# Kernel optimization log

Measured on AMD Instinct MI355X. Metric: run time of the kernel, lower is better.

The kernel has to match this reference:

```python
import jax, jax.numpy as jnp
import numpy as np

WIN = 3  # window_size (stride fixed to 1, matching module defaults)


def setup_inputs() -> dict:
    key = jax.random.key(0)
    ks = jax.random.split(key, 5)
    B, D, L = 4, 768, 4096
    s = 1.0 / np.sqrt(D)  # PyTorch nn.RNN init: U(-1/sqrt(hidden), 1/sqrt(hidden))
    return {
        "x": jax.random.normal(ks[0], (B, D, L), dtype=jnp.float32),
        "W_ih": jax.random.uniform(ks[1], (D, D), jnp.float32, -s, s),
        "W_hh": jax.random.uniform(ks[2], (D, D), jnp.float32, -s, s),
        "b_ih": jax.random.uniform(ks[3], (D,), jnp.float32, -s, s),
        "b_hh": jax.random.uniform(ks[4], (D,), jnp.float32, -s, s),
        "gamma": jnp.ones((L,), jnp.float32),  # LayerNorm over length axis
        "beta": jnp.zeros((L,), jnp.float32),
    }


def reference(x, W_ih, W_hh, b_ih, b_hh, gamma, beta):
    # x: [B, D, L]. For each position i, run a 1-layer ReLU RNN (h0=0) over the
    B, D, L = x.shape
    xt = jnp.transpose(x, (2, 0, 1))  # [L, B, D] (seq-first, like the torch code)
    xp = jnp.concatenate([jnp.zeros((WIN - 1, B, D), x.dtype), xt], axis=0)  # left-pad
    idx = jnp.arange(L)[:, None] + jnp.arange(WIN)[None, :]
    win = xp[idx]
    valid = (jnp.arange(L)[:, None] - (WIN - 1) + jnp.arange(WIN)[None, :]) >= 0

    def step(h, tw):
        x_t, m = tw  # x_t: [L, B, D], m: [L]
        hn = jax.nn.relu(x_t @ W_ih.T + b_ih + h @ W_hh.T + b_hh)
        # invalid (pre-window) steps keep h unchanged (stays 0) => exact short-window semantics
        return jnp.where(m[:, None, None], hn, h), None

    h0 = jnp.zeros((L, B, D), x.dtype)
    h, _ = jax.lax.scan(step, h0, (jnp.transpose(win, (1, 0, 2, 3)), valid.T))
    enc = jnp.transpose(h, (1, 2, 0))  # [B, D, L]

    # residual + LayerNorm with normalized_shape=(L,), eps=1e-12, affine (gamma=1, beta=0 at init)
    z = enc + x
    mean = jnp.mean(z, axis=-1, keepdims=True)
    var = jnp.var(z, axis=-1, keepdims=True)
    return (z - mean) / jnp.sqrt(var + 1e-12) * gamma + beta
```

## Files before the change

kernel.cpp:

```cpp
#include <hip/hip_runtime.h>

typedef unsigned short u16;
typedef __bf16 bf16x8 __attribute__((ext_vector_type(8)));
typedef float f32x4 __attribute__((ext_vector_type(4)));
typedef unsigned short u16x8 __attribute__((ext_vector_type(8)));

#define Bq 4
#define Dq 768
#define Lq 4096
#define Mq (Lq * Bq)

__device__ __forceinline__ u16 f2bf(float f) {
    unsigned int u = __builtin_bit_cast(unsigned int, f);
    u += 0x7fffu + ((u >> 16) & 1u);
    return (u16)(u >> 16);
}

__device__ __forceinline__ float bf2f(u16 h) {
    return __builtin_bit_cast(float, (unsigned int)h << 16);
}

__device__ __forceinline__ void async16(const void* g, void* l) {
    __builtin_amdgcn_global_load_lds(
        (const __attribute__((address_space(1))) unsigned int*)(unsigned long long)g,
        (__attribute__((address_space(3))) unsigned int*)(unsigned int)(unsigned long long)l,
        16, 0, 0);
}

__global__ __launch_bounds__(256) void prep_kernel(
    const float* __restrict__ Wih, const float* __restrict__ Whh,
    u16* __restrict__ Wihb, u16* __restrict__ Whhb,
    u16* __restrict__ Vpad, u16* __restrict__ Gpad) {
    int i = blockIdx.x * 256 + threadIdx.x;
    if (i < Dq * Dq) {
        Wihb[i] = f2bf(Wih[i]);
        Whhb[i] = f2bf(Whh[i]);
    }
    if (i < Bq * Dq) { Vpad[i] = 0; Gpad[i] = 0; }
}

__global__ __launch_bounds__(256) void transpose_kernel(
    const float* __restrict__ x, u16* __restrict__ Xt) {
    __shared__ u16 tile[64][66];
    int b = blockIdx.z, d0 = blockIdx.y * 64, l0 = blockIdx.x * 64;
    int tx = threadIdx.x & 63, ty = threadIdx.x >> 6;
    const float* xp = x + ((size_t)b * Dq + d0) * Lq + l0;
#pragma unroll
    for (int i = 0; i < 16; ++i) {
        int r = i * 4 + ty;
        tile[r][tx] = f2bf(xp[(size_t)r * Lq + tx]);
    }
    __syncthreads();
    u16* xt = Xt + ((size_t)l0 * Bq + b) * Dq + d0;
#pragma unroll
    for (int i = 0; i < 16; ++i) {
        int c = i * 4 + ty;
        xt[(size_t)c * Bq * Dq + tx] = tile[tx][c];
    }
}

template <int NSEG, int MODE>
__global__ __launch_bounds__(256) void gemm_kernel(
    const u16* __restrict__ A0, const u16* __restrict__ W0,
    const u16* __restrict__ A1, const u16* __restrict__ W1,
    u16* __restrict__ Out,
    const float* __restrict__ bih, const float* __restrict__ bhh) {
    __shared__ __align__(16) char smem[32768];
    u16* As0 = (u16*)smem;
    u16* As1 = As0 + 4096;
    u16* Bs0 = As0 + 8192;
    u16* Bs1 = As0 + 12288;

    int tid = threadIdx.x;
    int wave = tid >> 6, lane = tid & 63;
    int wr = wave >> 1, wc = wave & 1;
    int m0 = blockIdx.x * 128, n0 = blockIdx.y * 128;
    int lr = lane & 15, lq = lane >> 4;

    int srow = wave * 32 + (lane >> 2);
    int scol = (lane & 3) * 8;
    u16* lA0a = As0 + (wave * 32) * 32;
    u16* lA0b = As0 + (wave * 32 + 16) * 32;
    u16* lA1a = As1 + (wave * 32) * 32;
    u16* lA1b = As1 + (wave * 32 + 16) * 32;
    u16* lB0a = Bs0 + (wave * 32) * 32;
    u16* lB0b = Bs0 + (wave * 32 + 16) * 32;
    u16* lB1a = Bs1 + (wave * 32) * 32;
    u16* lB1b = Bs1 + (wave * 32 + 16) * 32;

    f32x4 acc[4][4];
#pragma unroll
    for (int i = 0; i < 4; ++i)
#pragma unroll
        for (int j = 0; j < 4; ++j) acc[i][j] = f32x4{0.f, 0.f, 0.f, 0.f};

#pragma unroll
    for (int seg = 0; seg < NSEG; ++seg) {
        const u16* Ab = (seg == 0) ? A0 : A1;
        const u16* Wb = (seg == 0) ? W0 : W1;
        const u16* ga = Ab + (size_t)(m0 + srow) * Dq + scol;
        const u16* gb = Wb + (size_t)(n0 + srow) * Dq + scol;

        for (int k0 = 0; k0 < Dq; k0 += 64) {
            async16(ga,               lA0a);
            async16(ga + 16 * Dq,     lA0b);
            async16(ga + 32,          lA1a);
            async16(ga + 16 * Dq + 32, lA1b);
            async16(gb,               lB0a);
            async16(gb + 16 * Dq,     lB0b);
            async16(gb + 32,          lB1a);
            async16(gb + 16 * Dq + 32, lB1b);
            ga += 64; gb += 64;
            __syncthreads();

#pragma unroll
            for (int s = 0; s < 2; ++s) {
                const u16* Asub = s ? As1 : As0;
                const u16* Bsub = s ? Bs1 : Bs0;
                bf16x8 af[4], bfr[4];
#pragma unroll
                for (int mt = 0; mt < 4; ++mt)
                    af[mt] = *(const bf16x8*)(Asub + (wr * 64 + mt * 16 + lr) * 32 + lq * 8);
#pragma unroll
                for (int nt = 0; nt < 4; ++nt)
                    bfr[nt] = *(const bf16x8*)(Bsub + (wc * 64 + nt * 16 + lr) * 32 + lq * 8);
#pragma unroll
                for (int mt = 0; mt < 4; ++mt)
#pragma unroll
                    for (int nt = 0; nt < 4; ++nt)
                        acc[mt][nt] = __builtin_amdgcn_mfma_f32_16x16x32_bf16(
                            af[mt], bfr[nt], acc[mt][nt], 0, 0, 0);
            }
            __syncthreads();
        }
    }

    if constexpr (MODE == 0) {
#pragma unroll
        for (int nt = 0; nt < 4; ++nt) {
            int gn = n0 + wc * 64 + nt * 16 + lr;
            float bsum = bih[gn] + bhh[gn];
#pragma unroll
            for (int mt = 0; mt < 4; ++mt) {
                int gm = m0 + wr * 64 + mt * 16 + lq * 4;
                f32x4 v = acc[mt][nt];
#pragma unroll
                for (int r = 0; r < 4; ++r)
                    Out[(size_t)(gm + r + Bq) * Dq + gn] = f2bf(fmaxf(v[r] + bsum, 0.f));
            }
        }
    } else {
        float* ep = (float*)smem;
        float* epw = ep + wave * (64 * 17);
        int l0w = (m0 >> 2) + wr * 16;
#pragma unroll
        for (int nt = 0; nt < 4; ++nt) {
            int gn = n0 + wc * 64 + nt * 16 + lr;
            float bsum = bih[gn] + bhh[gn];
#pragma unroll
            for (int mt = 0; mt < 4; ++mt) {
                int lmb = mt * 16 + lq * 4;
                f32x4 v = acc[mt][nt];
#pragma unroll
                for (int r = 0; r < 4; ++r)
                    epw[(lmb + r) * 17 + lr] = fmaxf(v[r] + bsum, 0.f);
            }
            __syncthreads();
            int bb = lane >> 4, cc = lane & 15;
            int gnc = n0 + wc * 64 + nt * 16 + cc;
            float vals[16];
#pragma unroll
            for (int ll = 0; ll < 16; ++ll)
                vals[ll] = epw[(ll * 4 + bb) * 17 + cc];
            u16* dst = Out + (size_t)bb * (Dq * Lq) + (size_t)gnc * Lq + l0w;
            u16x8 h0, h1;
#pragma unroll
            for (int j = 0; j < 8; ++j) { h0[j] = f2bf(vals[j]); h1[j] = f2bf(vals[8 + j]); }
            *(u16x8*)dst = h0;
            *(u16x8*)(dst + 8) = h1;
            __syncthreads();
        }
    }
}

__global__ __launch_bounds__(256) void ln_kernel(
    const u16* __restrict__ E, const float* __restrict__ x,
    const float* __restrict__ gamma, const float* __restrict__ beta,
    float* __restrict__ out) {
    __shared__ float red[2][4];
    size_t row = blockIdx.x;
    const u16x8* e8 = (const u16x8*)(E + row * Lq);
    const float* xr = x + row * Lq;
    float* o = out + row * Lq;
    int t = threadIdx.x;
    float z[16];
    float s = 0.f, sq = 0.f;
#pragma unroll
    for (int i = 0; i < 2; ++i) {
        int c = i * 256 + t;
        u16x8 ev = e8[c];
        f32x4 xv0 = *(const f32x4*)(xr + c * 8);
        f32x4 xv1 = *(const f32x4*)(xr + c * 8 + 4);
#pragma unroll
        for (int j = 0; j < 4; ++j) {
            float z0 = bf2f(ev[j]) + xv0[j];
            float z1 = bf2f(ev[4 + j]) + xv1[j];
            z[i * 8 + j] = z0;
            z[i * 8 + 4 + j] = z1;
            s += z0 + z1;
            sq += z0 * z0 + z1 * z1;
        }
    }
#pragma unroll
    for (int off = 32; off > 0; off >>= 1) {
        s += __shfl_down(s, off);
        sq += __shfl_down(sq, off);
    }
    int wave = t >> 6, lane = t & 63;
    if (lane == 0) { red[0][wave] = s; red[1][wave] = sq; }
    __syncthreads();
    s = red[0][0] + red[0][1] + red[0][2] + red[0][3];
    sq = red[1][0] + red[1][1] + red[1][2] + red[1][3];
    float mean = s * (1.f / Lq);
    float var = sq * (1.f / Lq) - mean * mean;
    float rstd = rsqrtf(var + 1e-12f);
#pragma unroll
    for (int i = 0; i < 2; ++i) {
        int c = i * 256 + t;
#pragma unroll
        for (int h = 0; h < 2; ++h) {
            int idx = c * 8 + h * 4;
            f32x4 gv = *(const f32x4*)(gamma + idx);
            f32x4 bv = *(const f32x4*)(beta + idx);
            f32x4 ov;
#pragma unroll
            for (int j = 0; j < 4; ++j)
                ov[j] = (z[i * 8 + h * 4 + j] - mean) * rstd * gv[j] + bv[j];
            *(f32x4*)(o + idx) = ov;
        }
    }
}

extern "C" void kernel_launch(void* const* d_in, const int* in_sizes, int n_in,
                              void* d_out, int out_size, void* d_ws, size_t ws_size,
                              hipStream_t stream) {
    const float* x     = (const float*)d_in[0];
    const float* Wih   = (const float*)d_in[1];
    const float* Whh   = (const float*)d_in[2];
    const float* bih   = (const float*)d_in[3];
    const float* bhh   = (const float*)d_in[4];
    const float* gamma = (const float*)d_in[5];
    const float* beta  = (const float*)d_in[6];
    float* out = (float*)d_out;

    char* ws = (char*)d_ws;
    u16* Xt    = (u16*)ws;   ws += (size_t)Mq * Dq * 2;
    u16* Wihb  = (u16*)ws;   ws += (size_t)Dq * Dq * 2;
    u16* Whhb  = (u16*)ws;   ws += (size_t)Dq * Dq * 2;
    u16* Vpad  = (u16*)ws;   ws += (size_t)(Mq + Bq) * Dq * 2;
    u16* Gpad  = (u16*)ws;   ws += (size_t)(Mq + Bq) * Dq * 2;
    u16* Eout  = (u16*)ws;   ws += (size_t)Mq * Dq * 2;

    prep_kernel<<<dim3((Dq * Dq + 255) / 256), 256, 0, stream>>>(
        Wih, Whh, Wihb, Whhb, Vpad, Gpad);
    transpose_kernel<<<dim3(Lq / 64, Dq / 64, Bq), 256, 0, stream>>>(x, Xt);

    dim3 ggrid(Mq / 128, Dq / 128);
    gemm_kernel<1, 0><<<ggrid, 256, 0, stream>>>(Xt, Wihb, nullptr, nullptr, Vpad, bih, bhh);
    gemm_kernel<2, 0><<<ggrid, 256, 0, stream>>>(Xt, Wihb, Vpad, Whhb, Gpad, bih, bhh);
    gemm_kernel<2, 1><<<ggrid, 256, 0, stream>>>(Xt, Wihb, Gpad, Whhb, Eout, bih, bhh);

    ln_kernel<<<dim3(Bq * Dq), 256, 0, stream>>>(Eout, x, gamma, beta, out);
}
```

Measured before the change: 275.1 us.

## Double-buffer GEMM LDS tiles with async prefetch and coalesce MODE-0 stores

Converts the GEMM main loop to a double-buffered pipeline: the next K-slice is loaded asynchronously into a second 32KB LDS buffer while MFMAs consume the current one, using explicit vmcnt waits and barriers. The two K segments are merged into one flat loop of 12*NSEG stages. The MODE-0 epilogue now stages bf16 results through LDS and writes 16-byte coalesced rows instead of scattered 2-byte stores. Dynamic LDS grows to 64KB per block, which may reduce occupancy.

```diff
diff --git a/kernel.cpp b/kernel.cpp
--- a/kernel.cpp
+++ b/kernel.cpp
@@ -65,11 +65,8 @@
     const u16* __restrict__ A1, const u16* __restrict__ W1,
     u16* __restrict__ Out,
     const float* __restrict__ bih, const float* __restrict__ bhh) {
-    __shared__ __align__(16) char smem[32768];
-    u16* As0 = (u16*)smem;
-    u16* As1 = As0 + 4096;
-    u16* Bs0 = As0 + 8192;
-    u16* Bs1 = As0 + 12288;
+    extern __shared__ __align__(16) char smem[];
+    const int NK = 12 * NSEG;
 
     int tid = threadIdx.x;
     int wave = tid >> 6, lane = tid & 63;
@@ -77,16 +74,25 @@
     int m0 = blockIdx.x * 128, n0 = blockIdx.y * 128;
     int lr = lane & 15, lq = lane >> 4;
 
-    int srow = wave * 32 + (lane >> 2);
-    int scol = (lane & 3) * 8;
-    u16* lA0a = As0 + (wave * 32) * 32;
-    u16* lA0b = As0 + (wave * 32 + 16) * 32;
-    u16* lA1a = As1 + (wave * 32) * 32;
-    u16* lA1b = As1 + (wave * 32 + 16) * 32;
-    u16* lB0a = Bs0 + (wave * 32) * 32;
-    u16* lB0b = Bs0 + (wave * 32 + 16) * 32;
-    u16* lB1a = Bs1 + (wave * 32) * 32;
-    u16* lB1b = Bs1 + (wave * 32 + 16) * 32;
+    size_t aoff = (size_t)(m0 + wave * 32 + (lane >> 2)) * Dq + (lane & 3) * 8;
+    size_t boff = (size_t)(n0 + wave * 32 + (lane >> 2)) * Dq + (lane & 3) * 8;
+    int ro = (wave * 32) * 32;
+
+    auto stage = [&](int j, char* buf) {
+        const u16* Ab = A0; const u16* Wb = W0; int kk = j;
+        if (NSEG == 2 && j >= 12) { Ab = A1; Wb = W1; kk = j - 12; }
+        const u16* ga = Ab + aoff + kk * 64;
+        const u16* gb = Wb + boff + kk * 64;
+        u16* s0 = (u16*)buf;
+        async16(ga,                s0 + ro);
+        async16(ga + 16 * Dq,      s0 + ro + 512);
+        async16(ga + 32,           s0 + 4096 + ro);
+        async16(ga + 16 * Dq + 32, s0 + 4096 + ro + 512);
+        async16(gb,                s0 + 8192 + ro);
+        async16(gb + 16 * Dq,      s0 + 8192 + ro + 512);
+        async16(gb + 32,           s0 + 12288 + ro);
+        async16(gb + 16 * Dq + 32, s0 + 12288 + ro + 512);
+    };
 
     f32x4 acc[4][4];
 #pragma unroll
@@ -94,60 +100,60 @@
 #pragma unroll
         for (int j = 0; j < 4; ++j) acc[i][j] = f32x4{0.f, 0.f, 0.f, 0.f};
 
-#pragma unroll
-    for (int seg = 0; seg < NSEG; ++seg) {
-        const u16* Ab = (seg == 0) ? A0 : A1;
-        const u16* Wb = (seg == 0) ? W0 : W1;
-        const u16* ga = Ab + (size_t)(m0 + srow) * Dq + scol;
-        const u16* gb = Wb + (size_t)(n0 + srow) * Dq + scol;
-
-        for (int k0 = 0; k0 < Dq; k0 += 64) {
-            async16(ga,               lA0a);
-            async16(ga + 16 * Dq,     lA0b);
-            async16(ga + 32,          lA1a);
-            async16(ga + 16 * Dq + 32, lA1b);
-            async16(gb,               lB0a);
-            async16(gb + 16 * Dq,     lB0b);
-            async16(gb + 32,          lB1a);
-            async16(gb + 16 * Dq + 32, lB1b);
-            ga += 64; gb += 64;
-            __syncthreads();
-
-#pragma unroll
-            for (int s = 0; s < 2; ++s) {
-                const u16* Asub = s ? As1 : As0;
-                const u16* Bsub = s ? Bs1 : Bs0;
-                bf16x8 af[4], bfr[4];
-#pragma unroll
-                for (int mt = 0; mt < 4; ++mt)
-                    af[mt] = *(const bf16x8*)(Asub + (wr * 64 + mt * 16 + lr) * 32 + lq * 8);
+    stage(0, smem);
+    for (int j = 0; j < NK; ++j) {
+        char* cur = smem + (size_t)(j & 1) * 32768;
+        if (j + 1 < NK) {
+            stage(j + 1, smem + (size_t)((j + 1) & 1) * 32768);
+            asm volatile("s_waitcnt vmcnt(8)\n\ts_barrier" ::: "memory");
+        } else {
+            asm volatile("s_waitcnt vmcnt(0)\n\ts_barrier" ::: "memory");
+        }
+
+        const u16* As = (const u16*)cur;
+#pragma unroll
+        for (int s = 0; s < 2; ++s) {
+            const u16* Asub = As + s * 4096;
+            const u16* Bsub = As + 8192 + s * 4096;
+            bf16x8 af[4], bfr[4];
+#pragma unroll
+            for (int mt = 0; mt < 4; ++mt)
+                af[mt] = *(const bf16x8*)(Asub + (wr * 64 + mt * 16 + lr) * 32 + lq * 8);
+#pragma unroll
+            for (int nt = 0; nt < 4; ++nt)
+                bfr[nt] = *(const bf16x8*)(Bsub + (wc * 64 + nt * 16 + lr) * 32 + lq * 8);
+#pragma unroll
+            for (int mt = 0; mt < 4; ++mt)
 #pragma unroll
                 for (int nt = 0; nt < 4; ++nt)
-                    bfr[nt] = *(const bf16x8*)(Bsub + (wc * 64 + nt * 16 + lr) * 32 + lq * 8);
-#pragma unroll
-                for (int mt = 0; mt < 4; ++mt)
-#pragma unroll
-                    for (int nt = 0; nt < 4; ++nt)
-                        acc[mt][nt] = __builtin_amdgcn_mfma_f32_16x16x32_bf16(
-                            af[mt], bfr[nt], acc[mt][nt], 0, 0, 0);
+                    acc[mt][nt] = __builtin_amdgcn_mfma_f32_16x16x32_bf16(
+                        af[mt], bfr[nt], acc[mt][nt], 0, 0, 0);
+        }
+        asm volatile("s_waitcnt lgkmcnt(0)\n\ts_barrier" ::: "memory");
+    }
+
+    if constexpr (MODE == 0) {
+        u16* tb = (u16*)smem;
+#pragma unroll
+        for (int nt = 0; nt < 4; ++nt) {
+            int cl = wc * 64 + nt * 16 + lr;
+            float bsum = bih[n0 + cl] + bhh[n0 + cl];
+#pragma unroll
+            for (int mt = 0; mt < 4; ++mt) {
+                int rl = wr * 64 + mt * 16 + lq * 4;
+                f32x4 v = acc[mt][nt];
+#pragma unroll
+                for (int r = 0; r < 4; ++r)
+                    tb[(rl + r) * 136 + cl] = f2bf(fmaxf(v[r] + bsum, 0.f));
             }
-            __syncthreads();
-        }
-    }
-
-    if constexpr (MODE == 0) {
-#pragma unroll
-        for (int nt = 0; nt < 4; ++nt) {
-            int gn = n0 + wc * 64 + nt * 16 + lr;
-            float bsum = bih[gn] + bhh[gn];
-#pragma unroll
-            for (int mt = 0; mt < 4; ++mt) {
-                int gm = m0 + wr * 64 + mt * 16 + lq * 4;
-                f32x4 v = acc[mt][nt];
-#pragma unroll
-                for (int r = 0; r < 4; ++r)
-                    Out[(size_t)(gm + r + Bq) * Dq + gn] = f2bf(fmaxf(v[r] + bsum, 0.f));
-            }
+        }
+        __syncthreads();
+        int rlane = tid & 15, rrow = tid >> 4;
+#pragma unroll
+        for (int s = 0; s < 8; ++s) {
+            int row = s * 16 + rrow;
+            u16x8 hv = *(const u16x8*)(tb + row * 136 + rlane * 8);
+            *(u16x8*)(Out + (size_t)(m0 + row + Bq) * Dq + n0 + rlane * 8) = hv;
         }
     } else {
         float* ep = (float*)smem;
@@ -175,7 +181,7 @@
             u16* dst = Out + (size_t)bb * (Dq * Lq) + (size_t)gnc * Lq + l0w;
             u16x8 h0, h1;
 #pragma unroll
-            for (int j = 0; j < 8; ++j) { h0[j] = f2bf(vals[j]); h1[j] = f2bf(vals[8 + j]); }
+            for (int k = 0; k < 8; ++k) { h0[k] = f2bf(vals[k]); h1[k] = f2bf(vals[8 + k]); }
             *(u16x8*)dst = h0;
             *(u16x8*)(dst + 8) = h1;
             __syncthreads();
@@ -266,9 +272,9 @@
     transpose_kernel<<<dim3(Lq / 64, Dq / 64, Bq), 256, 0, stream>>>(x, Xt);
 
     dim3 ggrid(Mq / 128, Dq / 128);
-    gemm_kernel<1, 0><<<ggrid, 256, 0, stream>>>(Xt, Wihb, nullptr, nullptr, Vpad, bih, bhh);
-    gemm_kernel<2, 0><<<ggrid, 256, 0, stream>>>(Xt, Wihb, Vpad, Whhb, Gpad, bih, bhh);
-    gemm_kernel<2, 1><<<ggrid, 256, 0, stream>>>(Xt, Wihb, Gpad, Whhb, Eout, bih, bhh);
+    gemm_kernel<1, 0><<<ggrid, 256, 65536, stream>>>(Xt, Wihb, nullptr, nullptr, Vpad, bih, bhh);
+    gemm_kernel<2, 0><<<ggrid, 256, 65536, stream>>>(Xt, Wihb, Vpad, Whhb, Gpad, bih, bhh);
+    gemm_kernel<2, 1><<<ggrid, 256, 65536, stream>>>(Xt, Wihb, Gpad, Whhb, Eout, bih, bhh);
 
     ln_kernel<<<dim3(Bq * Dq), 256, 0, stream>>>(Eout, x, gamma, beta, out);
 }
```

Measured after the change: 262.3 us. 1.05x faster.
